# Kernel optimization log

Measured on AMD Instinct MI355X. Metric: run time of the kernel, lower is better.

Reference implementation:

```python
import jax, jax.numpy as jnp
import numpy as np

N_NODES = 100000
N_EDGES = 1600000
IN_FEATS = 128
HIDDEN = 256
NUM_CLASSES = 1


def setup_inputs() -> dict:
    key = jax.random.key(0)
    ks = jax.random.split(key, 6)
    x = jax.random.normal(ks[0], (N_NODES, IN_FEATS), dtype=jnp.float32)
    src = jax.random.randint(ks[1], (N_EDGES,), 0, N_NODES, dtype=jnp.int64 if jax.config.jax_enable_x64 else jnp.int32).astype(jnp.int32)
    dst = jax.random.randint(ks[2], (N_EDGES,), 0, N_NODES, dtype=jnp.int32)
    W1 = jax.random.normal(ks[3], (IN_FEATS, HIDDEN), dtype=jnp.float32) * (1.0 / np.sqrt(IN_FEATS))
    b1 = jnp.zeros((HIDDEN,), dtype=jnp.float32)
    W2 = jax.random.normal(ks[4], (HIDDEN, NUM_CLASSES), dtype=jnp.float32) * (1.0 / np.sqrt(HIDDEN))
    b2 = jnp.zeros((NUM_CLASSES,), dtype=jnp.float32)
    return {"x": x, "src": src, "dst": dst, "W1": W1, "b1": b1, "W2": W2, "b2": b2}


def _graph_conv(x, src, dst, W, b):
    """DGL GraphConv with norm='both': D_out^{-1/2} gather -> scatter-add -> D_in^{-1/2}, then XW+b."""
    n = x.shape[0]
    ones = jnp.ones(src.shape[0], dtype=x.dtype)
    deg_out = jax.ops.segment_sum(ones, src, num_segments=n)
    deg_in = jax.ops.segment_sum(ones, dst, num_segments=n)
    norm_out = jax.lax.rsqrt(jnp.maximum(deg_out, 1.0))  # [N]
    norm_in = jax.lax.rsqrt(jnp.maximum(deg_in, 1.0))    # [N]
    h = x * norm_out[:, None]                 # [N, F]
    msg = h[src]                              # [E, F] gather (memory-bound)
    agg = jax.ops.segment_sum(msg, dst, num_segments=n)  # [N, F] scatter-add
    agg = agg * norm_in[:, None]
    return agg @ W + b


def reference(x, src, dst, W1, b1, W2, b2):
    # layer 0: GraphConv -> relu (dropout p=0.0 -> identity)
    h = jax.nn.relu(_graph_conv(x, src, dst, W1, b1))
    # output layer: GraphConv -> sigmoid
    h = jax.nn.sigmoid(_graph_conv(h, src, dst, W2, b2))
    return h
```

## Files before the change

kernel.cpp:

```cpp
#include <hip/hip_runtime.h>
#include <math.h>

#define NN 100000
#define NE 1600000
#define INF 128
#define HID 256
#define SCAN_BLK 256
#define NSCAN ((NN + SCAN_BLK - 1) / SCAN_BLK)
#define FGRP 8
#define FRNG (NN / FGRP)
#define NC 32
#define CHUNK (NE / NC)
#define HRNG 25000
#define MIDF (FGRP * NC)
#define MIDX 256
#define MIDW 5

typedef short bf16x8 __attribute__((ext_vector_type(8)));
typedef float f32x4 __attribute__((ext_vector_type(4)));

__device__ __forceinline__ unsigned int f2bf(float f) {
    unsigned int u = __float_as_uint(f);
    u = u + 0x7FFFu + ((u >> 16) & 1u);
    return u >> 16;
}

__launch_bounds__(1024)
__global__ void k_hist(const int* __restrict__ src, const int* __restrict__ dst,
                       unsigned int* __restrict__ hop, unsigned int* __restrict__ hip) {
    __shared__ unsigned int h[HRNG / 2];
    const int type = blockIdx.x & 1;
    const int gp = (blockIdx.x >> 1) & 3;
    const int c = blockIdx.x >> 3;
    const int lo = gp * HRNG;
    for (int i = threadIdx.x; i < HRNG / 2; i += 1024) h[i] = 0;
    __syncthreads();
    const int4* a4 = reinterpret_cast<const int4*>((type ? dst : src) + c * CHUNK);
    for (int k = threadIdx.x; k < CHUNK / 4; k += 1024) {
        int4 v = a4[k];
        int i0 = v.x - lo, i1 = v.y - lo, i2 = v.z - lo, i3 = v.w - lo;
        if ((unsigned)i0 < HRNG) atomicAdd(&h[i0 >> 1], 1u << ((i0 & 1) << 4));
        if ((unsigned)i1 < HRNG) atomicAdd(&h[i1 >> 1], 1u << ((i1 & 1) << 4));
        if ((unsigned)i2 < HRNG) atomicAdd(&h[i2 >> 1], 1u << ((i2 & 1) << 4));
        if ((unsigned)i3 < HRNG) atomicAdd(&h[i3 >> 1], 1u << ((i3 & 1) << 4));
    }
    __syncthreads();
    unsigned int* o = (type ? hip : hop) + (size_t)c * (NN / 2) + gp * (HRNG / 2);
    for (int i = threadIdx.x; i < HRNG / 2; i += 1024) o[i] = h[i];
}

__global__ void k_norms2(const unsigned int* __restrict__ hop, const unsigned int* __restrict__ hip,
                         float* __restrict__ nrm_out, float* __restrict__ nrm_in,
                         int* __restrict__ deg_in, int* __restrict__ partial) {
    __shared__ int sh[SCAN_BLK];
    int v = blockIdx.x * SCAN_BLK + threadIdx.x;
    int so = 0, si = 0;
    if (v < NN) {
        int w = v >> 1, sft = (v & 1) << 4;
        #pragma unroll
        for (int c = 0; c < NC; ++c) {
            so += (hop[(size_t)c * (NN / 2) + w] >> sft) & 0xFFFFu;
            si += (hip[(size_t)c * (NN / 2) + w] >> sft) & 0xFFFFu;
        }
        nrm_out[v] = rsqrtf(fmaxf((float)so, 1.0f));
        nrm_in[v]  = rsqrtf(fmaxf((float)si, 1.0f));
        deg_in[v]  = si;
    }
    sh[threadIdx.x] = si;
    __syncthreads();
    for (int off = SCAN_BLK / 2; off > 0; off >>= 1) {
        if (threadIdx.x < off) sh[threadIdx.x] += sh[threadIdx.x + off];
        __syncthreads();
    }
    if (threadIdx.x == 0) partial[blockIdx.x] = sh[0];
}

__global__ void k_scan2(int* __restrict__ partial) {
    int lane = threadIdx.x;
    int carry = 0;
    for (int c = 0; c < NSCAN; c += 64) {
        int idx = c + lane;
        int v = (idx < NSCAN) ? partial[idx] : 0;
        int s = v;
        #pragma unroll
        for (int off = 1; off < 64; off <<= 1) {
            int t = __shfl_up(s, off, 64);
            if (lane >= off) s += t;
        }
        if (idx < NSCAN) partial[idx] = s - v + carry;
        carry += __shfl(s, 63, 64);
    }
}

__global__ void k_scan3c(const int* __restrict__ deg_in, const int* __restrict__ partial,
                         int* __restrict__ offsets, const unsigned int* __restrict__ hip,
                         int* __restrict__ cbase) {
    __shared__ int sh[SCAN_BLK];
    int i = blockIdx.x * SCAN_BLK + threadIdx.x;
    int v = (i < NN) ? deg_in[i] : 0;
    sh[threadIdx.x] = v;
    __syncthreads();
    for (int off = 1; off < SCAN_BLK; off <<= 1) {
        int t = (threadIdx.x >= off) ? sh[threadIdx.x - off] : 0;
        __syncthreads();
        sh[threadIdx.x] += t;
        __syncthreads();
    }
    int ex = sh[threadIdx.x] - v + partial[blockIdx.x];
    if (i < NN) {
        offsets[i] = ex;
        int run = ex;
        int w = i >> 1, sft = (i & 1) << 4;
        #pragma unroll
        for (int c = 0; c < NC; ++c) {
            cbase[(size_t)c * NN + i] = run;
            run += (hip[(size_t)c * (NN / 2) + w] >> sft) & 0xFFFFu;
        }
    }
    if (i == 0) offsets[NN] = NE;
}

__launch_bounds__(1024)
__global__ void k_mid(const int* __restrict__ src, const int* __restrict__ dst,
                      const int* __restrict__ cbase, int* __restrict__ csr_src,
                      const float* __restrict__ x, const float* __restrict__ nrm_out,
                      unsigned int* __restrict__ xs,
                      const float* __restrict__ W1, const float* __restrict__ b1,
                      const float* __restrict__ W2, unsigned short* __restrict__ fragW,
                      float2* __restrict__ bw) {
    __shared__ int cur[FRNG];
    const int bid = blockIdx.x;
    if (bid < MIDF) {
        const int g = bid & (FGRP - 1);
        const int c = bid >> 3;
        const int lo = g * FRNG;
        const int* cb = cbase + (size_t)c * NN + lo;
        for (int i = threadIdx.x; i < FRNG; i += 1024) cur[i] = cb[i];
        __syncthreads();
        const int e0 = c * CHUNK;
        const int4* d4 = reinterpret_cast<const int4*>(dst + e0);
        for (int k = threadIdx.x; k < CHUNK / 4; k += 1024) {
            int4 v = d4[k];
            int e = e0 + k * 4;
            int i0 = v.x - lo, i1 = v.y - lo, i2 = v.z - lo, i3 = v.w - lo;
            if ((unsigned)i0 < FRNG) { int p = atomicAdd(&cur[i0], 1); csr_src[p] = src[e]; }
            if ((unsigned)i1 < FRNG) { int p = atomicAdd(&cur[i1], 1); csr_src[p] = src[e + 1]; }
            if ((unsigned)i2 < FRNG) { int p = atomicAdd(&cur[i2], 1); csr_src[p] = src[e + 2]; }
            if ((unsigned)i3 < FRNG) { int p = atomicAdd(&cur[i3], 1); csr_src[p] = src[e + 3]; }
        }
    } else if (bid < MIDF + MIDX) {
        const int nU2 = NN * (INF / 4);
        for (int i = (bid - MIDF) * 1024 + threadIdx.x; i < nU2; i += MIDX * 1024) {
            int row = i >> 5;
            float n = nrm_out[row];
            float4 v = *reinterpret_cast<const float4*>(x + (size_t)i * 4);
            uint2 r;
            r.x = f2bf(v.x * n) | (f2bf(v.y * n) << 16);
            r.y = f2bf(v.z * n) | (f2bf(v.w * n) << 16);
            *reinterpret_cast<uint2*>(xs + (size_t)i * 2) = r;
        }
    } else {
        int idx = (bid - MIDF - MIDX) * 1024 + threadIdx.x;
        if (idx < 4096) {
            int l = idx & 63, ks = (idx >> 6) & 3, nt = idx >> 8;
            int kbase = ks * 32 + ((l >> 4) << 3);
            int col = nt * 16 + (l & 15);
            bf16x8 r;
            #pragma unroll
            for (int i = 0; i < 8; ++i)
                r[i] = (short)f2bf(W1[(size_t)(kbase + i) * HID + col]);
            *reinterpret_cast<bf16x8*>(fragW + (size_t)idx * 8) = r;
        } else if (idx < 4096 + HID) {
            int n = idx - 4096;
            bw[n] = make_float2(b1[n], W2[n]);
        }
    }
}

__global__ void k_gather(const unsigned int* __restrict__ xs, const int* __restrict__ offsets,
                         const int* __restrict__ csr_src, const float* __restrict__ nrm_in,
                         unsigned int* __restrict__ aggb) {
    int row = blockIdx.x * 4 + (threadIdx.x >> 6);
    if (row >= NN) return;
    int lane = threadIdx.x & 63;
    int beg = offsets[row], end = offsets[row + 1];
    float a0 = 0.f, a1 = 0.f, b0 = 0.f, b1 = 0.f;
    float c0 = 0.f, c1 = 0.f, d0 = 0.f, d1 = 0.f;
    int j = beg;
    if (j + 4 <= end) {
        int s0 = csr_src[j], s1 = csr_src[j + 1], s2 = csr_src[j + 2], s3 = csr_src[j + 3];
        while (true) {
            unsigned int p0 = xs[(size_t)s0 * 64 + lane];
            unsigned int p1 = xs[(size_t)s1 * 64 + lane];
            unsigned int p2 = xs[(size_t)s2 * 64 + lane];
            unsigned int p3 = xs[(size_t)s3 * 64 + lane];
            j += 4;
            bool more = (j + 4 <= end);
            if (more) {
                s0 = csr_src[j]; s1 = csr_src[j + 1]; s2 = csr_src[j + 2]; s3 = csr_src[j + 3];
            }
            a0 += __uint_as_float(p0 << 16); a1 += __uint_as_float(p0 & 0xFFFF0000u);
            b0 += __uint_as_float(p1 << 16); b1 += __uint_as_float(p1 & 0xFFFF0000u);
            c0 += __uint_as_float(p2 << 16); c1 += __uint_as_float(p2 & 0xFFFF0000u);
            d0 += __uint_as_float(p3 << 16); d1 += __uint_as_float(p3 & 0xFFFF0000u);
            if (!more) break;
        }
    }
    for (; j < end; ++j) {
        unsigned int p0 = xs[(size_t)csr_src[j] * 64 + lane];
        a0 += __uint_as_float(p0 << 16);
        a1 += __uint_as_float(p0 & 0xFFFF0000u);
    }
    float ni = nrm_in[row];
    float lo = ((a0 + b0) + (c0 + d0)) * ni;
    float hi = ((a1 + b1) + (c1 + d1)) * ni;
    aggb[(size_t)row * 64 + lane] = f2bf(lo) | (f2bf(hi) << 16);
}

__launch_bounds__(256)
__global__ void k_gemm(const unsigned short* __restrict__ aggb,
                       const unsigned short* __restrict__ fragW,
                       const float2* __restrict__ bw, const float* __restrict__ nrm_out,
                       float* __restrict__ z) {
    const int l = threadIdx.x & 63;
    const int w = threadIdx.x >> 6;
    const int r0 = blockIdx.x * 64 + w * 16;
    const int n15 = l & 15;
    const int hi = l >> 4;
    const int arow = r0 + n15;

    bf16x8 a[4];
    if (arow < NN) {
        #pragma unroll
        for (int ks = 0; ks < 4; ++ks)
            a[ks] = *reinterpret_cast<const bf16x8*>(aggb + (size_t)arow * INF + ks * 32 + (hi << 3));
    } else {
        #pragma unroll
        for (int ks = 0; ks < 4; ++ks) a[ks] = (bf16x8){0, 0, 0, 0, 0, 0, 0, 0};
    }

    float pacc[4] = {0.f, 0.f, 0.f, 0.f};
    #pragma unroll
    for (int nt = 0; nt < 16; ++nt) {
        f32x4 acc = {0.f, 0.f, 0.f, 0.f};
        #pragma unroll
        for (int ks = 0; ks < 4; ++ks) {
            bf16x8 b = *reinterpret_cast<const bf16x8*>(fragW + (size_t)(((nt * 4 + ks) * 64 + l) << 3));
            acc = __builtin_amdgcn_mfma_f32_16x16x32_bf16(a[ks], b, acc, 0, 0, 0);
        }
        float2 c = bw[nt * 16 + n15];
        #pragma unroll
        for (int g = 0; g < 4; ++g)
            pacc[g] += fmaxf(acc[g] + c.x, 0.f) * c.y;
    }
    #pragma unroll
    for (int off = 1; off < 16; off <<= 1) {
        #pragma unroll
        for (int g = 0; g < 4; ++g) pacc[g] += __shfl_xor(pacc[g], off, 64);
    }
    if (n15 == 0) {
        #pragma unroll
        for (int g = 0; g < 4; ++g) {
            int gr = r0 + (hi << 2) + g;
            if (gr < NN) z[gr] = nrm_out[gr] * pacc[g];
        }
    }
}

__global__ void k_out(const float* __restrict__ z, const int* __restrict__ offsets,
                      const int* __restrict__ csr_src, const float* __restrict__ nrm_in,
                      const float* __restrict__ b2, float* __restrict__ out) {
    int v = blockIdx.x * 16 + (threadIdx.x >> 4);
    if (v >= NN) return;
    int li = threadIdx.x & 15;
    int beg = offsets[v], end = offsets[v + 1];
    float s = 0.f;
    for (int j = beg + li; j < end; j += 16) s += z[csr_src[j]];
    #pragma unroll
    for (int off = 1; off < 16; off <<= 1) s += __shfl_xor(s, off, 64);
    if (li == 0) {
        float val = s * nrm_in[v] + b2[0];
        out[v] = 1.0f / (1.0f + expf(-val));
    }
}

extern "C" void kernel_launch(void* const* d_in, const int* in_sizes, int n_in,
                              void* d_out, int out_size, void* d_ws, size_t ws_size,
                              hipStream_t stream) {
    const float* x   = (const float*)d_in[0];
    const int*   src = (const int*)d_in[1];
    const int*   dst = (const int*)d_in[2];
    const float* W1  = (const float*)d_in[3];
    const float* b1  = (const float*)d_in[4];
    const float* W2  = (const float*)d_in[5];
    const float* b2  = (const float*)d_in[6];
    float* out = (float*)d_out;

    int*   deg_in  = (int*)d_ws;
    int*   offsets = deg_in + NN;
    int*   partial = offsets + NN + 1;
    int*   csr_src = partial + NSCAN;
    float* nrm_out = (float*)(csr_src + NE);
    float* nrm_in  = nrm_out + NN;
    float* z       = nrm_in + NN;
    float2* bw     = (float2*)(z + NN);
    unsigned int* xs   = (unsigned int*)(bw + HID);
    unsigned int* aggb = xs + (size_t)NN * 64;
    unsigned short* fragW = (unsigned short*)(aggb + (size_t)NN * 64);
    unsigned int* hop = xs;
    unsigned int* hip = hop + (size_t)NC * (NN / 2);
    int* cbase = (int*)aggb;

    k_hist<<<2 * 4 * NC, 1024, 0, stream>>>(src, dst, hop, hip);
    k_norms2<<<NSCAN, SCAN_BLK, 0, stream>>>(hop, hip, nrm_out, nrm_in, deg_in, partial);
    k_scan2<<<1, 64, 0, stream>>>(partial);
    k_scan3c<<<NSCAN, SCAN_BLK, 0, stream>>>(deg_in, partial, offsets, hip, cbase);
    k_mid<<<MIDF + MIDX + MIDW, 1024, 0, stream>>>(src, dst, cbase, csr_src,
                                                   x, nrm_out, xs, W1, b1, W2, fragW, bw);
    k_gather<<<NN / 4, 256, 0, stream>>>(xs, offsets, csr_src, nrm_in, aggb);
    k_gemm<<<(NN + 63) / 64, 256, 0, stream>>>((const unsigned short*)aggb, fragW, bw, nrm_out, z);
    k_out<<<(NN + 15) / 16, 256, 0, stream>>>(z, offsets, csr_src, nrm_in, b2, out);
}
```

Baseline: 193.0 us.

## Split degree histogram into more unpacked blocks, move weight prep, add nontemporal gather access

The degree histogram now runs on 512 blocks, each covering an eighth of the node range. Counters are full 32-bit ints in LDS instead of packed 16-bit halves, and they are packed to 16 bits only when written out. This gives more parallelism and simpler atomics, at the cost of every block rescanning its chunk eight times instead of four. The W1 fragment and bias/W2 preparation moves from k_mid into the histogram kernel's extra blocks. k_gather now uses nontemporal loads for CSR indices and nontemporal stores for its output, to reduce cache pollution.

Measured after the change: 197.8 us. +2.5%, slower.

```diff
diff --git a/kernel.cpp b/kernel.cpp
--- a/kernel.cpp
+++ b/kernel.cpp
@@ -11,10 +11,9 @@
 #define FRNG (NN / FGRP)
 #define NC 32
 #define CHUNK (NE / NC)
-#define HRNG 25000
+#define HISTB 512
 #define MIDF (FGRP * NC)
 #define MIDX 256
-#define MIDW 5
 
 typedef short bf16x8 __attribute__((ext_vector_type(8)));
 typedef float f32x4 __attribute__((ext_vector_type(4)));
@@ -27,140 +26,34 @@
 
 __launch_bounds__(1024)
 __global__ void k_hist(const int* __restrict__ src, const int* __restrict__ dst,
-                       unsigned int* __restrict__ hop, unsigned int* __restrict__ hip) {
-    __shared__ unsigned int h[HRNG / 2];
-    const int type = blockIdx.x & 1;
-    const int gp = (blockIdx.x >> 1) & 3;
-    const int c = blockIdx.x >> 3;
-    const int lo = gp * HRNG;
-    for (int i = threadIdx.x; i < HRNG / 2; i += 1024) h[i] = 0;
-    __syncthreads();
-    const int4* a4 = reinterpret_cast<const int4*>((type ? dst : src) + c * CHUNK);
-    for (int k = threadIdx.x; k < CHUNK / 4; k += 1024) {
-        int4 v = a4[k];
-        int i0 = v.x - lo, i1 = v.y - lo, i2 = v.z - lo, i3 = v.w - lo;
-        if ((unsigned)i0 < HRNG) atomicAdd(&h[i0 >> 1], 1u << ((i0 & 1) << 4));
-        if ((unsigned)i1 < HRNG) atomicAdd(&h[i1 >> 1], 1u << ((i1 & 1) << 4));
-        if ((unsigned)i2 < HRNG) atomicAdd(&h[i2 >> 1], 1u << ((i2 & 1) << 4));
-        if ((unsigned)i3 < HRNG) atomicAdd(&h[i3 >> 1], 1u << ((i3 & 1) << 4));
-    }
-    __syncthreads();
-    unsigned int* o = (type ? hip : hop) + (size_t)c * (NN / 2) + gp * (HRNG / 2);
-    for (int i = threadIdx.x; i < HRNG / 2; i += 1024) o[i] = h[i];
-}
-
-__global__ void k_norms2(const unsigned int* __restrict__ hop, const unsigned int* __restrict__ hip,
-                         float* __restrict__ nrm_out, float* __restrict__ nrm_in,
-                         int* __restrict__ deg_in, int* __restrict__ partial) {
-    __shared__ int sh[SCAN_BLK];
-    int v = blockIdx.x * SCAN_BLK + threadIdx.x;
-    int so = 0, si = 0;
-    if (v < NN) {
-        int w = v >> 1, sft = (v & 1) << 4;
-        #pragma unroll
-        for (int c = 0; c < NC; ++c) {
-            so += (hop[(size_t)c * (NN / 2) + w] >> sft) & 0xFFFFu;
-            si += (hip[(size_t)c * (NN / 2) + w] >> sft) & 0xFFFFu;
-        }
-        nrm_out[v] = rsqrtf(fmaxf((float)so, 1.0f));
-        nrm_in[v]  = rsqrtf(fmaxf((float)si, 1.0f));
-        deg_in[v]  = si;
-    }
-    sh[threadIdx.x] = si;
-    __syncthreads();
-    for (int off = SCAN_BLK / 2; off > 0; off >>= 1) {
-        if (threadIdx.x < off) sh[threadIdx.x] += sh[threadIdx.x + off];
-        __syncthreads();
-    }
-    if (threadIdx.x == 0) partial[blockIdx.x] = sh[0];
-}
-
-__global__ void k_scan2(int* __restrict__ partial) {
-    int lane = threadIdx.x;
-    int carry = 0;
-    for (int c = 0; c < NSCAN; c += 64) {
-        int idx = c + lane;
-        int v = (idx < NSCAN) ? partial[idx] : 0;
-        int s = v;
-        #pragma unroll
-        for (int off = 1; off < 64; off <<= 1) {
-            int t = __shfl_up(s, off, 64);
-            if (lane >= off) s += t;
-        }
-        if (idx < NSCAN) partial[idx] = s - v + carry;
-        carry += __shfl(s, 63, 64);
-    }
-}
-
-__global__ void k_scan3c(const int* __restrict__ deg_in, const int* __restrict__ partial,
-                         int* __restrict__ offsets, const unsigned int* __restrict__ hip,
-                         int* __restrict__ cbase) {
-    __shared__ int sh[SCAN_BLK];
-    int i = blockIdx.x * SCAN_BLK + threadIdx.x;
-    int v = (i < NN) ? deg_in[i] : 0;
-    sh[threadIdx.x] = v;
-    __syncthreads();
-    for (int off = 1; off < SCAN_BLK; off <<= 1) {
-        int t = (threadIdx.x >= off) ? sh[threadIdx.x - off] : 0;
-        __syncthreads();
-        sh[threadIdx.x] += t;
-        __syncthreads();
-    }
-    int ex = sh[threadIdx.x] - v + partial[blockIdx.x];
-    if (i < NN) {
-        offsets[i] = ex;
-        int run = ex;
-        int w = i >> 1, sft = (i & 1) << 4;
-        #pragma unroll
-        for (int c = 0; c < NC; ++c) {
-            cbase[(size_t)c * NN + i] = run;
-            run += (hip[(size_t)c * (NN / 2) + w] >> sft) & 0xFFFFu;
-        }
-    }
-    if (i == 0) offsets[NN] = NE;
-}
-
-__launch_bounds__(1024)
-__global__ void k_mid(const int* __restrict__ src, const int* __restrict__ dst,
-                      const int* __restrict__ cbase, int* __restrict__ csr_src,
-                      const float* __restrict__ x, const float* __restrict__ nrm_out,
-                      unsigned int* __restrict__ xs,
-                      const float* __restrict__ W1, const float* __restrict__ b1,
-                      const float* __restrict__ W2, unsigned short* __restrict__ fragW,
-                      float2* __restrict__ bw) {
-    __shared__ int cur[FRNG];
+                       unsigned int* __restrict__ hop, unsigned int* __restrict__ hip,
+                       const float* __restrict__ W1, const float* __restrict__ b1,
+                       const float* __restrict__ W2, unsigned short* __restrict__ fragW,
+                       float2* __restrict__ bw) {
+    __shared__ int h[FRNG];
     const int bid = blockIdx.x;
-    if (bid < MIDF) {
-        const int g = bid & (FGRP - 1);
-        const int c = bid >> 3;
-        const int lo = g * FRNG;
-        const int* cb = cbase + (size_t)c * NN + lo;
-        for (int i = threadIdx.x; i < FRNG; i += 1024) cur[i] = cb[i];
-        __syncthreads();
-        const int e0 = c * CHUNK;
-        const int4* d4 = reinterpret_cast<const int4*>(dst + e0);
+    if (bid < HISTB) {
+        const int type = bid & 1;
+        const int gp = (bid >> 1) & 7;
+        const int c = bid >> 4;
+        const int lo = gp * FRNG;
+        for (int i = threadIdx.x; i < FRNG; i += 1024) h[i] = 0;
+        __syncthreads();
+        const int4* a4 = reinterpret_cast<const int4*>((type ? dst : src) + c * CHUNK);
         for (int k = threadIdx.x; k < CHUNK / 4; k += 1024) {
-            int4 v = d4[k];
-            int e = e0 + k * 4;
+            int4 v = a4[k];
             int i0 = v.x - lo, i1 = v.y - lo, i2 = v.z - lo, i3 = v.w - lo;
-            if ((unsigned)i0 < FRNG) { int p = atomicAdd(&cur[i0], 1); csr_src[p] = src[e]; }
-            if ((unsigned)i1 < FRNG) { int p = atomicAdd(&cur[i1], 1); csr_src[p] = src[e + 1]; }
-            if ((unsigned)i2 < FRNG) { int p = atomicAdd(&cur[i2], 1); csr_src[p] = src[e + 2]; }
-            if ((unsigned)i3 < FRNG) { int p = atomicAdd(&cur[i3], 1); csr_src[p] = src[e + 3]; }
-        }
-    } else if (bid < MIDF + MIDX) {
-        const int nU2 = NN * (INF / 4);
-        for (int i = (bid - MIDF) * 1024 + threadIdx.x; i < nU2; i += MIDX * 1024) {
-            int row = i >> 5;
-            float n = nrm_out[row];
-            float4 v = *reinterpret_cast<const float4*>(x + (size_t)i * 4);
-            uint2 r;
-            r.x = f2bf(v.x * n) | (f2bf(v.y * n) << 16);
-            r.y = f2bf(v.z * n) | (f2bf(v.w * n) << 16);
-            *reinterpret_cast<uint2*>(xs + (size_t)i * 2) = r;
-        }
+            if ((unsigned)i0 < FRNG) atomicAdd(&h[i0], 1);
+            if ((unsigned)i1 < FRNG) atomicAdd(&h[i1], 1);
+            if ((unsigned)i2 < FRNG) atomicAdd(&h[i2], 1);
+            if ((unsigned)i3 < FRNG) atomicAdd(&h[i3], 1);
+        }
+        __syncthreads();
+        unsigned int* o = (type ? hip : hop) + (size_t)c * (NN / 2) + gp * (FRNG / 2);
+        for (int i = threadIdx.x; i < FRNG / 2; i += 1024)
+            o[i] = (unsigned int)h[2 * i] | ((unsigned int)h[2 * i + 1] << 16);
     } else {
-        int idx = (bid - MIDF - MIDX) * 1024 + threadIdx.x;
+        int idx = (bid - HISTB) * 1024 + threadIdx.x;
         if (idx < 4096) {
             int l = idx & 63, ks = (idx >> 6) & 3, nt = idx >> 8;
             int kbase = ks * 32 + ((l >> 4) << 3);
@@ -177,6 +70,116 @@
     }
 }
 
+__global__ void k_norms2(const unsigned int* __restrict__ hop, const unsigned int* __restrict__ hip,
+                         float* __restrict__ nrm_out, float* __restrict__ nrm_in,
+                         int* __restrict__ deg_in, int* __restrict__ partial) {
+    __shared__ int sh[SCAN_BLK];
+    int v = blockIdx.x * SCAN_BLK + threadIdx.x;
+    int so = 0, si = 0;
+    if (v < NN) {
+        int w = v >> 1, sft = (v & 1) << 4;
+        #pragma unroll
+        for (int c = 0; c < NC; ++c) {
+            so += (hop[(size_t)c * (NN / 2) + w] >> sft) & 0xFFFFu;
+            si += (hip[(size_t)c * (NN / 2) + w] >> sft) & 0xFFFFu;
+        }
+        nrm_out[v] = rsqrtf(fmaxf((float)so, 1.0f));
+        nrm_in[v]  = rsqrtf(fmaxf((float)si, 1.0f));
+        deg_in[v]  = si;
+    }
+    sh[threadIdx.x] = si;
+    __syncthreads();
+    for (int off = SCAN_BLK / 2; off > 0; off >>= 1) {
+        if (threadIdx.x < off) sh[threadIdx.x] += sh[threadIdx.x + off];
+        __syncthreads();
+    }
+    if (threadIdx.x == 0) partial[blockIdx.x] = sh[0];
+}
+
+__global__ void k_scan2(int* __restrict__ partial) {
+    int lane = threadIdx.x;
+    int carry = 0;
+    for (int c = 0; c < NSCAN; c += 64) {
+        int idx = c + lane;
+        int v = (idx < NSCAN) ? partial[idx] : 0;
+        int s = v;
+        #pragma unroll
+        for (int off = 1; off < 64; off <<= 1) {
+            int t = __shfl_up(s, off, 64);
+            if (lane >= off) s += t;
+        }
+        if (idx < NSCAN) partial[idx] = s - v + carry;
+        carry += __shfl(s, 63, 64);
+    }
+}
+
+__global__ void k_scan3c(const int* __restrict__ deg_in, const int* __restrict__ partial,
+                         int* __restrict__ offsets, const unsigned int* __restrict__ hip,
+                         int* __restrict__ cbase) {
+    __shared__ int sh[SCAN_BLK];
+    int i = blockIdx.x * SCAN_BLK + threadIdx.x;
+    int v = (i < NN) ? deg_in[i] : 0;
+    sh[threadIdx.x] = v;
+    __syncthreads();
+    for (int off = 1; off < SCAN_BLK; off <<= 1) {
+        int t = (threadIdx.x >= off) ? sh[threadIdx.x - off] : 0;
+        __syncthreads();
+        sh[threadIdx.x] += t;
+        __syncthreads();
+    }
+    int ex = sh[threadIdx.x] - v + partial[blockIdx.x];
+    if (i < NN) {
+        offsets[i] = ex;
+        int run = ex;
+        int w = i >> 1, sft = (i & 1) << 4;
+        #pragma unroll
+        for (int c = 0; c < NC; ++c) {
+            cbase[(size_t)c * NN + i] = run;
+            run += (hip[(size_t)c * (NN / 2) + w] >> sft) & 0xFFFFu;
+        }
+    }
+    if (i == 0) offsets[NN] = NE;
+}
+
+__launch_bounds__(1024)
+__global__ void k_mid(const int* __restrict__ src, const int* __restrict__ dst,
+                      const int* __restrict__ cbase, int* __restrict__ csr_src,
+                      const float* __restrict__ x, const float* __restrict__ nrm_out,
+                      unsigned int* __restrict__ xs) {
+    __shared__ int cur[FRNG];
+    const int bid = blockIdx.x;
+    if (bid < MIDF) {
+        const int g = bid & (FGRP - 1);
+        const int c = bid >> 3;
+        const int lo = g * FRNG;
+        const int* cb = cbase + (size_t)c * NN + lo;
+        for (int i = threadIdx.x; i < FRNG; i += 1024) cur[i] = cb[i];
+        __syncthreads();
+        const int e0 = c * CHUNK;
+        const int4* d4 = reinterpret_cast<const int4*>(dst + e0);
+        for (int k = threadIdx.x; k < CHUNK / 4; k += 1024) {
+            int4 v = d4[k];
+            int e = e0 + k * 4;
+            int i0 = v.x - lo, i1 = v.y - lo, i2 = v.z - lo, i3 = v.w - lo;
+            if ((unsigned)i0 < FRNG) { int p = atomicAdd(&cur[i0], 1); csr_src[p] = src[e]; }
+            if ((unsigned)i1 < FRNG) { int p = atomicAdd(&cur[i1], 1); csr_src[p] = src[e + 1]; }
+            if ((unsigned)i2 < FRNG) { int p = atomicAdd(&cur[i2], 1); csr_src[p] = src[e + 2]; }
+            if ((unsigned)i3 < FRNG) { int p = atomicAdd(&cur[i3], 1); csr_src[p] = src[e + 3]; }
+        }
+    } else {
+        const int nU2 = NN * (INF / 4);
+        for (int i = (bid - MIDF) * 1024 + threadIdx.x; i < nU2; i += MIDX * 1024) {
+            int row = i >> 5;
+            float n = nrm_out[row];
+            float4 v = *reinterpret_cast<const float4*>(x + (size_t)i * 4);
+            uint2 r;
+            r.x = f2bf(v.x * n) | (f2bf(v.y * n) << 16);
+            r.y = f2bf(v.z * n) | (f2bf(v.w * n) << 16);
+            *reinterpret_cast<uint2*>(xs + (size_t)i * 2) = r;
+        }
+    }
+}
+
 __global__ void k_gather(const unsigned int* __restrict__ xs, const int* __restrict__ offsets,
                          const int* __restrict__ csr_src, const float* __restrict__ nrm_in,
                          unsigned int* __restrict__ aggb) {
@@ -188,7 +191,10 @@
     float c0 = 0.f, c1 = 0.f, d0 = 0.f, d1 = 0.f;
     int j = beg;
     if (j + 4 <= end) {
-        int s0 = csr_src[j], s1 = csr_src[j + 1], s2 = csr_src[j + 2], s3 = csr_src[j + 3];
+        int s0 = __builtin_nontemporal_load(csr_src + j);
+        int s1 = __builtin_nontemporal_load(csr_src + j + 1);
+        int s2 = __builtin_nontemporal_load(csr_src + j + 2);
+        int s3 = __builtin_nontemporal_load(csr_src + j + 3);
         while (true) {
             unsigned int p0 = xs[(size_t)s0 * 64 + lane];
             unsigned int p1 = xs[(size_t)s1 * 64 + lane];
@@ -197,7 +203,10 @@
             j += 4;
             bool more = (j + 4 <= end);
             if (more) {
-                s0 = csr_src[j]; s1 = csr_src[j + 1]; s2 = csr_src[j + 2]; s3 = csr_src[j + 3];
+                s0 = __builtin_nontemporal_load(csr_src + j);
+                s1 = __builtin_nontemporal_load(csr_src + j + 1);
+                s2 = __builtin_nontemporal_load(csr_src + j + 2);
+                s3 = __builtin_nontemporal_load(csr_src + j + 3);
             }
             a0 += __uint_as_float(p0 << 16); a1 += __uint_as_float(p0 & 0xFFFF0000u);
             b0 += __uint_as_float(p1 << 16); b1 += __uint_as_float(p1 & 0xFFFF0000u);
@@ -214,7 +223,7 @@
     float ni = nrm_in[row];
     float lo = ((a0 + b0) + (c0 + d0)) * ni;
     float hi = ((a1 + b1) + (c1 + d1)) * ni;
-    aggb[(size_t)row * 64 + lane] = f2bf(lo) | (f2bf(hi) << 16);
+    __builtin_nontemporal_store(f2bf(lo) | (f2bf(hi) << 16), aggb + (size_t)row * 64 + lane);
 }
 
 __launch_bounds__(256)
@@ -311,12 +320,11 @@
     unsigned int* hip = hop + (size_t)NC * (NN / 2);
     int* cbase = (int*)aggb;
 
-    k_hist<<<2 * 4 * NC, 1024, 0, stream>>>(src, dst, hop, hip);
+    k_hist<<<HISTB + 5, 1024, 0, stream>>>(src, dst, hop, hip, W1, b1, W2, fragW, bw);
     k_norms2<<<NSCAN, SCAN_BLK, 0, stream>>>(hop, hip, nrm_out, nrm_in, deg_in, partial);
     k_scan2<<<1, 64, 0, stream>>>(partial);
     k_scan3c<<<NSCAN, SCAN_BLK, 0, stream>>>(deg_in, partial, offsets, hip, cbase);
-    k_mid<<<MIDF + MIDX + MIDW, 1024, 0, stream>>>(src, dst, cbase, csr_src,
-                                                   x, nrm_out, xs, W1, b1, W2, fragW, bw);
+    k_mid<<<MIDF + MIDX, 1024, 0, stream>>>(src, dst, cbase, csr_src, x, nrm_out, xs);
     k_gather<<<NN / 4, 256, 0, stream>>>(xs, offsets, csr_src, nrm_in, aggb);
     k_gemm<<<(NN + 63) / 64, 256, 0, stream>>>((const unsigned short*)aggb, fragW, bw, nrm_out, z);
     k_out<<<(NN + 15) / 16, 256, 0, stream>>>(z, offsets, csr_src, nrm_in, b2, out);
```
